# Kernel tuning notes

Hardware: AMD Instinct MI355X
Metric: run time of the kernel (lower is better)

## Reference

```python
import jax, jax.numpy as jnp
import numpy as np

B, S, D = 1, 2048, 2048
H, KV, HD = 32, 8, 64          # heads, kv heads, head_dim
WINDOW = 1024                  # sliding window (left), causal
ROPE_THETA = 10000.0


def setup_inputs() -> dict:
    key = jax.random.key(0)
    ks = jax.random.split(key, 5)
    scale = 1.0 / np.sqrt(D)
    x = jax.random.normal(ks[0], (B, S, D), dtype=jnp.float32)
    wq = jax.random.normal(ks[1], (D, H * HD), dtype=jnp.float32) * scale
    wk = jax.random.normal(ks[2], (D, KV * HD), dtype=jnp.float32) * scale
    wv = jax.random.normal(ks[3], (D, KV * HD), dtype=jnp.float32) * scale
    wo = jax.random.normal(ks[4], (H * HD, D), dtype=jnp.float32) * scale
    # RoPE frequencies: freqs_cis = exp(i * t * theta^{-2j/hd}), stored as cos/sin
    inv_freq = 1.0 / (ROPE_THETA ** (np.arange(0, HD, 2, dtype=np.float32) / HD))  # [HD/2]
    t = np.arange(S, dtype=np.float32)
    ang = np.outer(t, inv_freq)  # [S, HD/2]
    freqs_cos = jnp.asarray(np.cos(ang), dtype=jnp.float32)
    freqs_sin = jnp.asarray(np.sin(ang), dtype=jnp.float32)
    return {"x": x, "wq": wq, "wk": wk, "wv": wv, "wo": wo,
            "freqs_cos": freqs_cos, "freqs_sin": freqs_sin}


def _apply_rope(t, cos, sin):
    # t: [B,S,h,HD]; pairs (t[...,2i], t[...,2i+1]) form complex numbers
    tr = t.reshape(*t.shape[:-1], HD // 2, 2)
    a, b = tr[..., 0], tr[..., 1]
    c = cos[None, :, None, :]  # [1,S,1,HD/2]
    s = sin[None, :, None, :]
    ra = a * c - b * s
    rb = a * s + b * c
    return jnp.stack([ra, rb], axis=-1).reshape(t.shape)


def reference(x, wq, wk, wv, wo, freqs_cos, freqs_sin):
    q = (x @ wq).reshape(B, S, H, HD)
    k = (x @ wk).reshape(B, S, KV, HD)
    v = (x @ wv).reshape(B, S, KV, HD)
    q = _apply_rope(q, freqs_cos, freqs_sin)
    k = _apply_rope(k, freqs_cos, freqs_sin)
    # GQA: repeat kv heads to match query heads
    k = jnp.repeat(k, H // KV, axis=2)  # [B,S,H,HD]
    v = jnp.repeat(v, H // KV, axis=2)
    scale = jnp.asarray(1.0 / np.sqrt(HD), dtype=x.dtype)
    scores = jnp.einsum('bqhd,bkhd->bhqk', q, k) * scale  # [B,H,S,S]
    i = jnp.arange(S)[:, None]
    j = jnp.arange(S)[None, :]
    allowed = (j <= i) & (j >= i - WINDOW)  # causal + sliding window
    scores = jnp.where(allowed[None, None], scores, jnp.asarray(-1e30, dtype=scores.dtype))
    attn = jax.nn.softmax(scores, axis=-1)
    out = jnp.einsum('bhqk,bkhd->bqhd', attn, v).reshape(B, S, H * HD)
    return out @ wo
```

## Files before the change

kernel.cpp:

```cpp
#include <hip/hip_runtime.h>
#include <stdint.h>

typedef __bf16 bf16_t;
typedef __bf16 bf16x8 __attribute__((ext_vector_type(8)));
typedef __bf16 bf16x4 __attribute__((ext_vector_type(4)));
typedef float floatx4 __attribute__((ext_vector_type(4)));

#define AS3(p) ((__attribute__((address_space(3))) void*)(p))
#define AS1(p) ((__attribute__((address_space(1))) void*)(void*)(p))

__global__ __launch_bounds__(256) void prep_k(const float* __restrict__ x,
                                              const float* __restrict__ wq,
                                              const float* __restrict__ wk,
                                              const float* __restrict__ wv,
                                              const float* __restrict__ wo,
                                              bf16_t* __restrict__ xb,
                                              bf16_t* __restrict__ wt) {
  __shared__ __align__(16) bf16_t T[64][68];
  const int b = blockIdx.x;
  const int t = threadIdx.x;
  if (b < 2048) {
    const int i = (b * 256 + t) * 8;
    floatx4 a = *(const floatx4*)&x[i];
    floatx4 c = *(const floatx4*)&x[i + 4];
    bf16x8 o;
#pragma unroll
    for (int j = 0; j < 4; ++j) { o[j] = (bf16_t)a[j]; o[4 + j] = (bf16_t)c[j]; }
    *(bf16x8*)&xb[i] = o;
    return;
  }
  int b2 = b - 2048;
  const float* src;
  int ncols, bx, by;
  bf16_t* dst;
  if (b2 < 1024) {
    src = wq; ncols = 2048; dst = wt; bx = b2 & 31; by = b2 >> 5;
  } else if (b2 < 1280) {
    const int i2 = b2 - 1024;
    src = wk; ncols = 512; dst = wt + (size_t)2048 * 2048; bx = i2 & 7; by = i2 >> 3;
  } else if (b2 < 1536) {
    const int i2 = b2 - 1280;
    src = wv; ncols = 512; dst = wt + (size_t)2560 * 2048; bx = i2 & 7; by = i2 >> 3;
  } else {
    const int i2 = b2 - 1536;
    src = wo; ncols = 2048; dst = wt + (size_t)3072 * 2048; bx = i2 & 31; by = i2 >> 5;
  }
  const int nt = bx * 64, kt = by * 64;
  const int r0 = t >> 4;
  const int c0 = (t & 15) << 2;
#pragma unroll
  for (int p = 0; p < 4; ++p) {
    const int row = p * 16 + r0;
    floatx4 v = *(const floatx4*)&src[(size_t)(kt + row) * ncols + nt + c0];
    bf16x4 bb;
#pragma unroll
    for (int i = 0; i < 4; ++i) bb[i] = (bf16_t)v[i];
    *(bf16x4*)&T[row][c0] = bb;
  }
  __syncthreads();
#pragma unroll
  for (int p = 0; p < 4; ++p) {
    const int n = p * 16 + r0;
    bf16x4 tmp;
#pragma unroll
    for (int i = 0; i < 4; ++i) tmp[i] = T[c0 + i][n];
    *(bf16x4*)&dst[(size_t)(nt + n) * 2048 + kt + c0] = tmp;
  }
}

template <int EPI>
__global__ __launch_bounds__(256) void gemm_k(const bf16_t* __restrict__ A,
                                              const bf16_t* __restrict__ Bt,
                                              bf16_t* __restrict__ o0,
                                              bf16_t* __restrict__ o1,
                                              bf16_t* __restrict__ o2,
                                              float* __restrict__ fo,
                                              const float* __restrict__ fcos,
                                              const float* __restrict__ fsin) {
  constexpr int K = 2048;
  __shared__ __align__(16) bf16_t As[64 * 128];
  __shared__ __align__(16) bf16_t Bs[128 * 128];
  const int tid = threadIdx.x;
  const int lane = tid & 63;
  const int w = tid >> 6;
  const int quad = lane >> 4;
  const int l15 = lane & 15;

  const int nx = gridDim.x, ny = gridDim.y;
  const int flat = blockIdx.y * nx + blockIdx.x;
  const int xcd = flat & 7;
  const int c = flat >> 3;
  const int CW = nx >> 1, CH = ny >> 2;
  const int bx = (xcd & 1) * CW + (c % CW);
  const int by = (xcd >> 1) * CH + (c / CW);
  const int m0 = by * 64;
  const int n0 = bx * 128;

  const int sr4 = lane >> 4;
  const int ch = lane & 15;
  const int ce = ch ^ sr4;
  const int codd = ch ^ (sr4 + 4);
  const bf16_t* gAe = A + (size_t)(m0 + w * 16 + sr4) * K + ce * 8;
  const bf16_t* gAo = A + (size_t)(m0 + w * 16 + sr4) * K + codd * 8;
  const bf16_t* gBe = Bt + (size_t)(n0 + w * 32 + sr4) * K + ce * 8;
  const bf16_t* gBo = Bt + (size_t)(n0 + w * 32 + sr4) * K + codd * 8;
  bf16_t* lA = &As[w * 2048];
  bf16_t* lB = &Bs[w * 4096];
  floatx4 acc[4][2] = {};

  for (int k0 = 0; k0 < K; k0 += 128) {
#pragma unroll
    for (int j = 0; j < 4; ++j)
      __builtin_amdgcn_global_load_lds(AS1(((j & 1) ? gAo : gAe) + (size_t)j * 4 * K + k0),
                                       AS3(lA + j * 512), 16, 0, 0);
#pragma unroll
    for (int j = 0; j < 8; ++j)
      __builtin_amdgcn_global_load_lds(AS1(((j & 1) ? gBo : gBe) + (size_t)j * 4 * K + k0),
                                       AS3(lB + j * 512), 16, 0, 0);
    __syncthreads();
#pragma unroll
    for (int kk = 0; kk < 4; ++kk) {
      const int co = ((kk * 4 + quad) ^ (l15 & 7)) << 3;
      bf16x8 af[4], bfr[2];
#pragma unroll
      for (int i = 0; i < 4; ++i) af[i] = *(const bf16x8*)&As[(i * 16 + l15) * 128 + co];
#pragma unroll
      for (int i = 0; i < 2; ++i)
        bfr[i] = *(const bf16x8*)&Bs[(w * 32 + i * 16 + l15) * 128 + co];
#pragma unroll
      for (int mi = 0; mi < 4; ++mi)
#pragma unroll
        for (int ni = 0; ni < 2; ++ni)
          acc[mi][ni] =
              __builtin_amdgcn_mfma_f32_16x16x32_bf16(af[mi], bfr[ni], acc[mi][ni], 0, 0, 0);
    }
    __syncthreads();
  }

  if constexpr (EPI == 0) {
#pragma unroll
    for (int ni = 0; ni < 2; ++ni) {
      const int col = n0 + w * 32 + ni * 16 + l15;
#pragma unroll
      for (int mi = 0; mi < 4; ++mi) {
        const int sb = m0 + mi * 16 + quad * 4;
        if (col < 2560) {
          const int fi = (col & 63) >> 1;
#pragma unroll
          for (int r = 0; r < 4; ++r) {
            const float v = acc[mi][ni][r];
            const float prt = __shfl_xor(v, 1);
            const int s = sb + r;
            const float cc = fcos[s * 32 + fi];
            const float sn = fsin[s * 32 + fi];
            const float ov = (col & 1) ? (prt * sn + v * cc) : (v * cc - prt * sn);
            if (col < 2048)
              o0[(size_t)s * 2048 + col] = (bf16_t)ov;
            else
              o1[(size_t)s * 512 + (col - 2048)] = (bf16_t)ov;
          }
        } else {
          const int sp = (sb & ~31) | (quad * 8 + (mi & 1) * 4);
          bf16x4 pv;
#pragma unroll
          for (int r = 0; r < 4; ++r) pv[r] = (bf16_t)acc[mi][ni][r];
          *(bf16x4*)&o2[(size_t)(col - 2560) * 2048 + sp] = pv;
        }
      }
    }
  } else {
#pragma unroll
    for (int ni = 0; ni < 2; ++ni) {
      const int col = n0 + w * 32 + ni * 16 + l15;
#pragma unroll
      for (int mi = 0; mi < 4; ++mi) {
        const int sb = m0 + mi * 16 + quad * 4;
#pragma unroll
        for (int r = 0; r < 4; ++r) fo[(size_t)(sb + r) * 2048 + col] = acc[mi][ni][r];
      }
    }
  }
}

__global__ __launch_bounds__(256) void attn_k(const bf16_t* __restrict__ qb_,
                                              const bf16_t* __restrict__ kb_,
                                              const bf16_t* __restrict__ vt_,
                                              bf16_t* __restrict__ ob_) {
  __shared__ __align__(16) bf16_t sm[2][8 * 512];
  const int lane = threadIdx.x & 63, w = threadIdx.x >> 6;
  const int quad = lane >> 4, l15 = lane & 15;
  const int h = blockIdx.y, g = h >> 2;
  const int qb = (gridDim.x - 1 - blockIdx.x) * 64;
  const int qw = qb + w * 16;
  const int q = qw + l15;
  const bf16_t* qrow = qb_ + (size_t)q * 2048 + h * 64;
  const bf16x8 qf0 = *(const bf16x8*)(qrow + quad * 8);
  const bf16x8 qf1 = *(const bf16x8*)(qrow + 32 + quad * 8);
  floatx4 acc0 = {}, acc1 = {}, acc2 = {}, acc3 = {}, accl = {};
  const float SC = 0.125f * 1.44269504088896340736f;
  bf16x8 ones;
#pragma unroll
  for (int i = 0; i < 8; ++i) ones[i] = (bf16_t)1.0f;

  int kbB = qb - 1024;
  if (kbB < 0) kbB = 0;
  kbB &= ~31;
  const int nT = (qb + 64 - kbB) >> 5;
  int myS = qw - 1024;
  if (myS < 0) myS = 0;
  myS &= ~31;
  const int myE = qw + 16;

  const int lr = lane & 15, lc = lane >> 4;
  const bf16_t* gk = kb_ + (size_t)(kbB + (w >> 1) * 16 + lr) * 512 + g * 64 +
                     ((w & 1) * 4 + lc) * 8;
  const bf16_t* gv = vt_ + (size_t)(g * 64 + w * 16 + lr) * 2048 + kbB + lc * 8;

#define STAGE(bi, ti)                                                              \
  do {                                                                             \
    __builtin_amdgcn_global_load_lds(AS1(gk + (size_t)(ti) * (32 * 512)),          \
                                     AS3(&sm[bi][w * 512]), 16, 0, 0);             \
    __builtin_amdgcn_global_load_lds(AS1(gv + (size_t)(ti) * 32),                  \
                                     AS3(&sm[bi][(4 + w) * 512]), 16, 0, 0);       \
  } while (0)

#define MSK(pv, key)                                        \
  do {                                                      \
    if ((key) > q || (key) + 1024 < q) pv = -1.0e30f;       \
  } while (0)

  int kb = kbB;
  STAGE(0, 0);
  __syncthreads();
  for (int i = 0; i < nT; ++i, kb += 32) {
    if (i + 1 < nT) STAGE((i + 1) & 1, i + 1);
    if (kb >= myS && kb < myE) {
      const bf16_t* base = &sm[i & 1][(size_t)lane * 8];
      const bf16x8 k0 = *(const bf16x8*)(base);
      const bf16x8 k1 = *(const bf16x8*)(base + 512);
      const bf16x8 k2 = *(const bf16x8*)(base + 1024);
      const bf16x8 k3 = *(const bf16x8*)(base + 1536);
      const bf16x8 v0 = *(const bf16x8*)(base + 2048);
      const bf16x8 v1 = *(const bf16x8*)(base + 2560);
      const bf16x8 v2 = *(const bf16x8*)(base + 3072);
      const bf16x8 v3 = *(const bf16x8*)(base + 3584);
      floatx4 z0 = {}, z1 = {};
      z0 = __builtin_amdgcn_mfma_f32_16x16x32_bf16(k0, qf0, z0, 0, 0, 0);
      z0 = __builtin_amdgcn_mfma_f32_16x16x32_bf16(k1, qf1, z0, 0, 0, 0);
      z1 = __builtin_amdgcn_mfma_f32_16x16x32_bf16(k2, qf0, z1, 0, 0, 0);
      z1 = __builtin_amdgcn_mfma_f32_16x16x32_bf16(k3, qf1, z1, 0, 0, 0);
      float p0 = z0[0] * SC - 32.0f, p1 = z0[1] * SC - 32.0f;
      float p2 = z0[2] * SC - 32.0f, p3 = z0[3] * SC - 32.0f;
      float p4 = z1[0] * SC - 32.0f, p5 = z1[1] * SC - 32.0f;
      float p6 = z1[2] * SC - 32.0f, p7 = z1[3] * SC - 32.0f;
      if ((kb + 31 > qw) || (kb < qw - 1009)) {
        const int kq = kb + quad * 4;
        MSK(p0, kq + 0); MSK(p1, kq + 1); MSK(p2, kq + 2); MSK(p3, kq + 3);
        MSK(p4, kq + 16); MSK(p5, kq + 17); MSK(p6, kq + 18); MSK(p7, kq + 19);
      }
      bf16x8 pf;
      pf[0] = (bf16_t)__builtin_amdgcn_exp2f(p0);
      pf[1] = (bf16_t)__builtin_amdgcn_exp2f(p1);
      pf[2] = (bf16_t)__builtin_amdgcn_exp2f(p2);
      pf[3] = (bf16_t)__builtin_amdgcn_exp2f(p3);
      pf[4] = (bf16_t)__builtin_amdgcn_exp2f(p4);
      pf[5] = (bf16_t)__builtin_amdgcn_exp2f(p5);
      pf[6] = (bf16_t)__builtin_amdgcn_exp2f(p6);
      pf[7] = (bf16_t)__builtin_amdgcn_exp2f(p7);
      accl = __builtin_amdgcn_mfma_f32_16x16x32_bf16(ones, pf, accl, 0, 0, 0);
      acc0 = __builtin_amdgcn_mfma_f32_16x16x32_bf16(v0, pf, acc0, 0, 0, 0);
      acc1 = __builtin_amdgcn_mfma_f32_16x16x32_bf16(v1, pf, acc1, 0, 0, 0);
      acc2 = __builtin_amdgcn_mfma_f32_16x16x32_bf16(v2, pf, acc2, 0, 0, 0);
      acc3 = __builtin_amdgcn_mfma_f32_16x16x32_bf16(v3, pf, acc3, 0, 0, 0);
    }
    __syncthreads();
  }
#undef STAGE
#undef MSK

  const float inv = 1.0f / accl[0];
  bf16_t* obase = ob_ + (size_t)q * 2048 + h * 64 + quad * 4;
  bf16x4 ov;
#pragma unroll
  for (int r = 0; r < 4; ++r) ov[r] = (bf16_t)(acc0[r] * inv);
  *(bf16x4*)(obase) = ov;
#pragma unroll
  for (int r = 0; r < 4; ++r) ov[r] = (bf16_t)(acc1[r] * inv);
  *(bf16x4*)(obase + 16) = ov;
#pragma unroll
  for (int r = 0; r < 4; ++r) ov[r] = (bf16_t)(acc2[r] * inv);
  *(bf16x4*)(obase + 32) = ov;
#pragma unroll
  for (int r = 0; r < 4; ++r) ov[r] = (bf16_t)(acc3[r] * inv);
  *(bf16x4*)(obase + 48) = ov;
}

extern "C" void kernel_launch(void* const* d_in, const int* in_sizes, int n_in, void* d_out,
                              int out_size, void* d_ws, size_t ws_size, hipStream_t stream) {
  (void)in_sizes;
  (void)n_in;
  (void)out_size;
  (void)ws_size;
  const float* x = (const float*)d_in[0];
  const float* wq = (const float*)d_in[1];
  const float* wk = (const float*)d_in[2];
  const float* wv = (const float*)d_in[3];
  const float* wo = (const float*)d_in[4];
  const float* fcos = (const float*)d_in[5];
  const float* fsin = (const float*)d_in[6];
  float* out = (float*)d_out;

  bf16_t* xb = (bf16_t*)d_ws;
  bf16_t* wt = xb + (size_t)2048 * 2048;
  bf16_t* qbuf = wt + (size_t)5120 * 2048;
  bf16_t* kbuf = qbuf + (size_t)2048 * 2048;
  bf16_t* vtb = kbuf + (size_t)2048 * 512;
  bf16_t* att = vtb + (size_t)512 * 2048;

  prep_k<<<4608, 256, 0, stream>>>(x, wq, wk, wv, wo, xb, wt);
  gemm_k<0><<<dim3(24, 32), 256, 0, stream>>>(xb, wt, qbuf, kbuf, vtb, nullptr, fcos, fsin);
  attn_k<<<dim3(32, 32), 256, 0, stream>>>(qbuf, kbuf, vtb, att);
  gemm_k<1><<<dim3(16, 32), 256, 0, stream>>>(att, wt + (size_t)3072 * 2048, nullptr, nullptr,
                                              nullptr, out, fcos, fsin);
}
```

Measured before the change: 201.9 us.

## Shrink GEMM K-tile to 64 and load attention K/V directly from global

The GEMM kernel's K-step drops from 128 to 64, which halves its LDS tiles and changes the swizzled global-to-LDS load mapping. The attention kernel drops its double-buffered LDS staging and block-wide barriers, and each wave now reads K and V fragments straight from global memory over only its own key range. This removes barrier synchronisation and the shared-loop overhead of waves whose windows differ. In exchange, K/V reuse across the four waves now relies on cache instead of LDS, the global loads are not prefetched, and the GEMM does twice as many barrier iterations.

```diff
diff --git a/kernel.cpp b/kernel.cpp
--- a/kernel.cpp
+++ b/kernel.cpp
@@ -78,8 +78,8 @@
                                               const float* __restrict__ fcos,
                                               const float* __restrict__ fsin) {
   constexpr int K = 2048;
-  __shared__ __align__(16) bf16_t As[64 * 128];
-  __shared__ __align__(16) bf16_t Bs[128 * 128];
+  __shared__ __align__(16) bf16_t As[64 * 64];
+  __shared__ __align__(16) bf16_t Bs[128 * 64];
   const int tid = threadIdx.x;
   const int lane = tid & 63;
   const int w = tid >> 6;
@@ -96,37 +96,31 @@
   const int m0 = by * 64;
   const int n0 = bx * 128;
 
-  const int sr4 = lane >> 4;
-  const int ch = lane & 15;
-  const int ce = ch ^ sr4;
-  const int codd = ch ^ (sr4 + 4);
-  const bf16_t* gAe = A + (size_t)(m0 + w * 16 + sr4) * K + ce * 8;
-  const bf16_t* gAo = A + (size_t)(m0 + w * 16 + sr4) * K + codd * 8;
-  const bf16_t* gBe = Bt + (size_t)(n0 + w * 32 + sr4) * K + ce * 8;
-  const bf16_t* gBo = Bt + (size_t)(n0 + w * 32 + sr4) * K + codd * 8;
-  bf16_t* lA = &As[w * 2048];
-  bf16_t* lB = &Bs[w * 4096];
+  const int sr = lane >> 3;
+  const int sc = ((lane & 7) ^ (sr & 7)) << 3;
+  const bf16_t* gA = A + (size_t)(m0 + w * 16 + sr) * K + sc;
+  const bf16_t* gB = Bt + (size_t)(n0 + w * 32 + sr) * K + sc;
+  bf16_t* lA = &As[w * 1024];
+  bf16_t* lB = &Bs[w * 2048];
   floatx4 acc[4][2] = {};
 
-  for (int k0 = 0; k0 < K; k0 += 128) {
-#pragma unroll
-    for (int j = 0; j < 4; ++j)
-      __builtin_amdgcn_global_load_lds(AS1(((j & 1) ? gAo : gAe) + (size_t)j * 4 * K + k0),
-                                       AS3(lA + j * 512), 16, 0, 0);
-#pragma unroll
-    for (int j = 0; j < 8; ++j)
-      __builtin_amdgcn_global_load_lds(AS1(((j & 1) ? gBo : gBe) + (size_t)j * 4 * K + k0),
-                                       AS3(lB + j * 512), 16, 0, 0);
+  for (int k0 = 0; k0 < K; k0 += 64) {
+    __builtin_amdgcn_global_load_lds(AS1(gA + k0), AS3(lA), 16, 0, 0);
+    __builtin_amdgcn_global_load_lds(AS1(gA + 8 * K + k0), AS3(lA + 512), 16, 0, 0);
+#pragma unroll
+    for (int qq = 0; qq < 4; ++qq)
+      __builtin_amdgcn_global_load_lds(AS1(gB + (size_t)qq * 8 * K + k0),
+                                       AS3(lB + qq * 512), 16, 0, 0);
     __syncthreads();
 #pragma unroll
-    for (int kk = 0; kk < 4; ++kk) {
+    for (int kk = 0; kk < 2; ++kk) {
       const int co = ((kk * 4 + quad) ^ (l15 & 7)) << 3;
       bf16x8 af[4], bfr[2];
 #pragma unroll
-      for (int i = 0; i < 4; ++i) af[i] = *(const bf16x8*)&As[(i * 16 + l15) * 128 + co];
+      for (int i = 0; i < 4; ++i) af[i] = *(const bf16x8*)&As[(i * 16 + l15) * 64 + co];
 #pragma unroll
       for (int i = 0; i < 2; ++i)
-        bfr[i] = *(const bf16x8*)&Bs[(w * 32 + i * 16 + l15) * 128 + co];
+        bfr[i] = *(const bf16x8*)&Bs[(w * 32 + i * 16 + l15) * 64 + co];
 #pragma unroll
       for (int mi = 0; mi < 4; ++mi)
 #pragma unroll
@@ -186,7 +180,6 @@
                                               const bf16_t* __restrict__ kb_,
                                               const bf16_t* __restrict__ vt_,
                                               bf16_t* __restrict__ ob_) {
-  __shared__ __align__(16) bf16_t sm[2][8 * 512];
   const int lane = threadIdx.x & 63, w = threadIdx.x >> 6;
   const int quad = lane >> 4, l15 = lane & 15;
   const int h = blockIdx.y, g = h >> 2;
@@ -202,80 +195,59 @@
 #pragma unroll
   for (int i = 0; i < 8; ++i) ones[i] = (bf16_t)1.0f;
 
-  int kbB = qb - 1024;
-  if (kbB < 0) kbB = 0;
-  kbB &= ~31;
-  const int nT = (qb + 64 - kbB) >> 5;
   int myS = qw - 1024;
   if (myS < 0) myS = 0;
   myS &= ~31;
   const int myE = qw + 16;
 
-  const int lr = lane & 15, lc = lane >> 4;
-  const bf16_t* gk = kb_ + (size_t)(kbB + (w >> 1) * 16 + lr) * 512 + g * 64 +
-                     ((w & 1) * 4 + lc) * 8;
-  const bf16_t* gv = vt_ + (size_t)(g * 64 + w * 16 + lr) * 2048 + kbB + lc * 8;
-
-#define STAGE(bi, ti)                                                              \
-  do {                                                                             \
-    __builtin_amdgcn_global_load_lds(AS1(gk + (size_t)(ti) * (32 * 512)),          \
-                                     AS3(&sm[bi][w * 512]), 16, 0, 0);             \
-    __builtin_amdgcn_global_load_lds(AS1(gv + (size_t)(ti) * 32),                  \
-                                     AS3(&sm[bi][(4 + w) * 512]), 16, 0, 0);       \
-  } while (0)
+  const bf16_t* gk = kb_ + (size_t)l15 * 512 + g * 64 + quad * 8;
+  const bf16_t* gv = vt_ + (size_t)(g * 64 + l15) * 2048 + quad * 8;
 
 #define MSK(pv, key)                                        \
   do {                                                      \
     if ((key) > q || (key) + 1024 < q) pv = -1.0e30f;       \
   } while (0)
 
-  int kb = kbB;
-  STAGE(0, 0);
-  __syncthreads();
-  for (int i = 0; i < nT; ++i, kb += 32) {
-    if (i + 1 < nT) STAGE((i + 1) & 1, i + 1);
-    if (kb >= myS && kb < myE) {
-      const bf16_t* base = &sm[i & 1][(size_t)lane * 8];
-      const bf16x8 k0 = *(const bf16x8*)(base);
-      const bf16x8 k1 = *(const bf16x8*)(base + 512);
-      const bf16x8 k2 = *(const bf16x8*)(base + 1024);
-      const bf16x8 k3 = *(const bf16x8*)(base + 1536);
-      const bf16x8 v0 = *(const bf16x8*)(base + 2048);
-      const bf16x8 v1 = *(const bf16x8*)(base + 2560);
-      const bf16x8 v2 = *(const bf16x8*)(base + 3072);
-      const bf16x8 v3 = *(const bf16x8*)(base + 3584);
-      floatx4 z0 = {}, z1 = {};
-      z0 = __builtin_amdgcn_mfma_f32_16x16x32_bf16(k0, qf0, z0, 0, 0, 0);
-      z0 = __builtin_amdgcn_mfma_f32_16x16x32_bf16(k1, qf1, z0, 0, 0, 0);
-      z1 = __builtin_amdgcn_mfma_f32_16x16x32_bf16(k2, qf0, z1, 0, 0, 0);
-      z1 = __builtin_amdgcn_mfma_f32_16x16x32_bf16(k3, qf1, z1, 0, 0, 0);
-      float p0 = z0[0] * SC - 32.0f, p1 = z0[1] * SC - 32.0f;
-      float p2 = z0[2] * SC - 32.0f, p3 = z0[3] * SC - 32.0f;
-      float p4 = z1[0] * SC - 32.0f, p5 = z1[1] * SC - 32.0f;
-      float p6 = z1[2] * SC - 32.0f, p7 = z1[3] * SC - 32.0f;
-      if ((kb + 31 > qw) || (kb < qw - 1009)) {
-        const int kq = kb + quad * 4;
-        MSK(p0, kq + 0); MSK(p1, kq + 1); MSK(p2, kq + 2); MSK(p3, kq + 3);
-        MSK(p4, kq + 16); MSK(p5, kq + 17); MSK(p6, kq + 18); MSK(p7, kq + 19);
-      }
-      bf16x8 pf;
-      pf[0] = (bf16_t)__builtin_amdgcn_exp2f(p0);
-      pf[1] = (bf16_t)__builtin_amdgcn_exp2f(p1);
-      pf[2] = (bf16_t)__builtin_amdgcn_exp2f(p2);
-      pf[3] = (bf16_t)__builtin_amdgcn_exp2f(p3);
-      pf[4] = (bf16_t)__builtin_amdgcn_exp2f(p4);
-      pf[5] = (bf16_t)__builtin_amdgcn_exp2f(p5);
-      pf[6] = (bf16_t)__builtin_amdgcn_exp2f(p6);
-      pf[7] = (bf16_t)__builtin_amdgcn_exp2f(p7);
-      accl = __builtin_amdgcn_mfma_f32_16x16x32_bf16(ones, pf, accl, 0, 0, 0);
-      acc0 = __builtin_amdgcn_mfma_f32_16x16x32_bf16(v0, pf, acc0, 0, 0, 0);
-      acc1 = __builtin_amdgcn_mfma_f32_16x16x32_bf16(v1, pf, acc1, 0, 0, 0);
-      acc2 = __builtin_amdgcn_mfma_f32_16x16x32_bf16(v2, pf, acc2, 0, 0, 0);
-      acc3 = __builtin_amdgcn_mfma_f32_16x16x32_bf16(v3, pf, acc3, 0, 0, 0);
-    }
-    __syncthreads();
-  }
-#undef STAGE
+  for (int kb = myS; kb < myE; kb += 32) {
+    const bf16_t* kbase = gk + (size_t)kb * 512;
+    const bf16x8 k0 = *(const bf16x8*)(kbase);
+    const bf16x8 k1 = *(const bf16x8*)(kbase + 32);
+    const bf16x8 k2 = *(const bf16x8*)(kbase + 16 * 512);
+    const bf16x8 k3 = *(const bf16x8*)(kbase + 16 * 512 + 32);
+    const bf16_t* vbase = gv + kb;
+    const bf16x8 v0 = *(const bf16x8*)(vbase);
+    const bf16x8 v1 = *(const bf16x8*)(vbase + 16 * 2048);
+    const bf16x8 v2 = *(const bf16x8*)(vbase + 32 * 2048);
+    const bf16x8 v3 = *(const bf16x8*)(vbase + 48 * 2048);
+    floatx4 z0 = {}, z1 = {};
+    z0 = __builtin_amdgcn_mfma_f32_16x16x32_bf16(k0, qf0, z0, 0, 0, 0);
+    z0 = __builtin_amdgcn_mfma_f32_16x16x32_bf16(k1, qf1, z0, 0, 0, 0);
+    z1 = __builtin_amdgcn_mfma_f32_16x16x32_bf16(k2, qf0, z1, 0, 0, 0);
+    z1 = __builtin_amdgcn_mfma_f32_16x16x32_bf16(k3, qf1, z1, 0, 0, 0);
+    float p0 = z0[0] * SC - 32.0f, p1 = z0[1] * SC - 32.0f;
+    float p2 = z0[2] * SC - 32.0f, p3 = z0[3] * SC - 32.0f;
+    float p4 = z1[0] * SC - 32.0f, p5 = z1[1] * SC - 32.0f;
+    float p6 = z1[2] * SC - 32.0f, p7 = z1[3] * SC - 32.0f;
+    if ((kb + 31 > qw) || (kb < qw - 1009)) {
+      const int kq = kb + quad * 4;
+      MSK(p0, kq + 0); MSK(p1, kq + 1); MSK(p2, kq + 2); MSK(p3, kq + 3);
+      MSK(p4, kq + 16); MSK(p5, kq + 17); MSK(p6, kq + 18); MSK(p7, kq + 19);
+    }
+    bf16x8 pf;
+    pf[0] = (bf16_t)__builtin_amdgcn_exp2f(p0);
+    pf[1] = (bf16_t)__builtin_amdgcn_exp2f(p1);
+    pf[2] = (bf16_t)__builtin_amdgcn_exp2f(p2);
+    pf[3] = (bf16_t)__builtin_amdgcn_exp2f(p3);
+    pf[4] = (bf16_t)__builtin_amdgcn_exp2f(p4);
+    pf[5] = (bf16_t)__builtin_amdgcn_exp2f(p5);
+    pf[6] = (bf16_t)__builtin_amdgcn_exp2f(p6);
+    pf[7] = (bf16_t)__builtin_amdgcn_exp2f(p7);
+    accl = __builtin_amdgcn_mfma_f32_16x16x32_bf16(ones, pf, accl, 0, 0, 0);
+    acc0 = __builtin_amdgcn_mfma_f32_16x16x32_bf16(v0, pf, acc0, 0, 0, 0);
+    acc1 = __builtin_amdgcn_mfma_f32_16x16x32_bf16(v1, pf, acc1, 0, 0, 0);
+    acc2 = __builtin_amdgcn_mfma_f32_16x16x32_bf16(v2, pf, acc2, 0, 0, 0);
+    acc3 = __builtin_amdgcn_mfma_f32_16x16x32_bf16(v3, pf, acc3, 0, 0, 0);
+  }
 #undef MSK
 
   const float inv = 1.0f / accl[0];
```

After: 286.6 us. 41.9% more time.
